# Performance work log

Hardware: AMD Instinct MI355X
Metric: run time of the kernel (lower is better)

## Reference

```python
import jax, jax.numpy as jnp
import numpy as np

B, S, F, D, H, L, NSUB, DFF = 64, 128, 62, 256, 4, 6, 32, 512
DH = D // 2           # each attention branch works on half of d_model
DEPTH = DH // H       # per-head dim = 32
NEG = -1000000000.0


def _rescale(w):
    # (1+e) / (1+exp(1-w))
    e1 = jnp.exp(jnp.float32(1.0))
    return (1.0 + e1) / (1.0 + jnp.exp(1.0 - w))


def _ln(x, g, b):
    mu = jnp.mean(x, -1, keepdims=True)
    v = jnp.var(x, -1, keepdims=True)
    return (x - mu) / jnp.sqrt(v + 1e-6) * g + b


def _heads(x, W, b):
    bsz, s, _ = x.shape
    return (x @ W + b).reshape(bsz, s, H, DEPTH).transpose(0, 2, 1, 3)  # (B,H,S,depth)


def setup_inputs():
    key = jax.random.key(0)
    ks = list(jax.random.split(key, 16))
    it = iter(ks)
    n = lambda shape: jax.random.normal(next(it), shape, jnp.float32) * 0.02
    inp = {
        "x": jax.random.normal(next(it), (B, S, F), jnp.float32),
        "adj_matrix": jax.random.normal(next(it), (B, S, S), jnp.float32),
        "dist_matrix": jax.random.uniform(next(it), (B, S, S), jnp.float32) * 10.0,
        "atom_match_matrix": jax.random.uniform(next(it), (B, NSUB, S), jnp.float32),
        "sum_atoms": jnp.ones((B, NSUB, 1), jnp.float32),
        "emb_W": n((F, D)), "emb_b": jnp.zeros((D,), jnp.float32),
        "glob_W": n((D, D)), "glob_b": jnp.zeros((D,), jnp.float32),
    }
    # per-layer params, stacked along leading L axis for lax.scan
    for p in ["Wq1", "Wk1", "Wv1", "Wo1", "Wq2", "Wk2", "Wv2", "Wo2"]:
        inp[p] = n((L, DH, DH))
    for p in ["bq1", "bk1", "bv1", "bo1", "bq2", "bk2", "bv2", "bo2"]:
        inp[p] = jnp.zeros((L, DH), jnp.float32)
    inp["Wf1"] = n((L, D, DFF)); inp["bf1"] = jnp.zeros((L, DFF), jnp.float32)
    inp["Wf2"] = n((L, DFF, D)); inp["bf2"] = jnp.zeros((L, D), jnp.float32)
    inp["g1"] = jnp.ones((L, D), jnp.float32); inp["be1"] = jnp.zeros((L, D), jnp.float32)
    inp["g2"] = jnp.ones((L, D), jnp.float32); inp["be2"] = jnp.zeros((L, D), jnp.float32)
    return inp


def reference(x, adj_matrix, dist_matrix, atom_match_matrix, sum_atoms,
              emb_W, emb_b, glob_W, glob_b,
              Wq1, Wk1, Wv1, Wo1, Wq2, Wk2, Wv2, Wo2,
              bq1, bk1, bv1, bo1, bq2, bk2, bv2, bo2,
              Wf1, bf1, Wf2, bf2, g1, be1, g2, be2):
    # padding mask from raw atom features: (B,1,1,S)
    mask = (jnp.sum(x, -1) == 0).astype(jnp.float32)[:, None, None, :]
    adj = adj_matrix[:, None]                  # (B,1,S,S) additive bias
    dist = _rescale(dist_matrix)[:, None]      # (B,1,S,S) multiplicative bias
    scale = 1.0 / jnp.sqrt(jnp.float32(DEPTH))

    h = jax.nn.relu(x @ emb_W + emb_b)         # embedding (eval mode, no dropout)

    def layer(h, p):
        (wq1, wk1, wv1, wo1, wq2, wk2, wv2, wo2,
         bq1_, bk1_, bv1_, bo1_, bq2_, bk2_, bv2_, bo2_,
         wf1, bf1_, wf2, bf2_, gg1, bb1, gg2, bb2) = p
        x1, x2 = jnp.split(h, 2, axis=-1)
        # local branch: plain scaled dot product + mask + adjacency bias
        Q = _heads(x1, wq1, bq1_); K = _heads(x1, wk1, bk1_); V = _heads(x1, wv1, bv1_)
        s = jnp.einsum('bhid,bhjd->bhij', Q, K) * scale + mask * NEG + adj
        o = jnp.einsum('bhij,bhjd->bhid', jax.nn.softmax(s, -1), V)
        x_l = o.transpose(0, 2, 1, 3).reshape(h.shape[0], S, DH) @ wo1 + bo1_
        # global branch: relu(QK^T) * rescaled_dist * scale + mask
        Q = _heads(x2, wq2, bq2_); K = _heads(x2, wk2, bk2_); V = _heads(x2, wv2, bv2_)
        s = jax.nn.relu(jnp.einsum('bhid,bhjd->bhij', Q, K)) * dist * scale + mask * NEG
        o = jnp.einsum('bhij,bhjd->bhid', jax.nn.softmax(s, -1), V)
        x_g = o.transpose(0, 2, 1, 3).reshape(h.shape[0], S, DH) @ wo2 + bo2_
        attn = jnp.concatenate([x_l, x_g], -1)
        out1 = _ln(h + attn, gg1, bb1)
        ffn = jax.nn.gelu(out1 @ wf1 + bf1_, approximate=False) @ wf2 + bf2_
        return _ln(ffn + out1, gg2, bb2), None

    xs = (Wq1, Wk1, Wv1, Wo1, Wq2, Wk2, Wv2, Wo2,
          bq1, bk1, bv1, bo1, bq2, bk2, bv2, bo2,
          Wf1, bf1, Wf2, bf2, g1, be1, g2, be2)
    h, _ = jax.lax.scan(layer, h, xs)

    pooled = (atom_match_matrix @ h) / sum_atoms      # (B,NSUB,D)
    out = jax.nn.relu(pooled @ glob_W + glob_b)
    return out
```

## Files before the change

kernel.cpp:

```cpp
#include <hip/hip_runtime.h>
#include <math.h>

#define B_ 64
#define S_ 128
#define F_ 62
#define D_ 256
#define H_ 4
#define L_ 6
#define NSUB_ 32
#define DFF_ 512
#define DH_ 128
#define DEPTH_ 32
#define MS_ (B_*S_)
#define NEGV (-1000000000.0f)
#define SCALE_ 0.17677669529663687f

typedef unsigned short u16;
typedef __attribute__((ext_vector_type(8))) short short8;
typedef __attribute__((ext_vector_type(4))) float f32x4;

__device__ __forceinline__ u16 f2b(float f){
  unsigned u = __float_as_uint(f);
  unsigned r = (u + 0x7fffu + ((u >> 16) & 1u)) >> 16;
  return (u16)r;
}

__device__ __forceinline__ void glds16(const void* g, void* l){
  __builtin_amdgcn_global_load_lds(
      (const __attribute__((address_space(1))) unsigned int*)g,
      (__attribute__((address_space(3))) unsigned int*)l, 16, 0, 0);
}

__global__ __launch_bounds__(256) void adjrescale_kernel(
    const float* __restrict__ adj, const float* __restrict__ dist,
    const float* __restrict__ maskb,
    float* __restrict__ adjm, float* __restrict__ distr){
  size_t i = (size_t)blockIdx.x*256 + threadIdx.x;
  int j = (int)(i & (S_-1));
  int b = (int)(i >> 14);
  const float e1 = 2.718281828459045f;
  distr[i] = (1.0f + e1) / (1.0f + expf(1.0f - dist[i])) * SCALE_;
  adjm[i]  = adj[i] + maskb[b*S_ + j];
}

struct TD { const float* src; u16* dst; int K, N, L; };
struct TDs { TD d[11]; };
__global__ __launch_bounds__(256) void transpose_all_kernel(TDs a){
  const TD p = a.d[blockIdx.z];
  int n0 = blockIdx.x*32, k0 = blockIdx.y*32;
  if(n0 >= p.N || k0 >= p.K) return;
  __shared__ float tbuf[32][33];
  int tx = threadIdx.x, ty = threadIdx.y;
  for(int l = 0; l < p.L; l++){
    const float* src = p.src + (size_t)l*p.K*p.N;
    u16* dst = p.dst + (size_t)l*p.K*p.N;
    #pragma unroll
    for(int i = 0; i < 4; i++)
      tbuf[ty + i*8][tx] = src[(size_t)(k0 + ty + i*8)*p.N + n0 + tx];
    __syncthreads();
    #pragma unroll
    for(int i = 0; i < 4; i++)
      dst[(size_t)(n0 + ty + i*8)*p.K + k0 + tx] = f2b(tbuf[tx][ty + i*8]);
    __syncthreads();
  }
}

__global__ __launch_bounds__(256) void embed_kernel(const float* __restrict__ x,
    const float* __restrict__ W, const float* __restrict__ bias,
    float* __restrict__ h, u16* __restrict__ h_bf, float* __restrict__ maskb){
  __shared__ float xs[4][F_];
  int r0 = blockIdx.x*4;
  int t = threadIdx.x;
  if(t < 4*F_){ int rr = t / F_, ff = t - rr*F_; xs[rr][ff] = x[(size_t)(r0+rr)*F_ + ff]; }
  __syncthreads();
  if(t < 4){
    float s = 0.f;
    #pragma unroll
    for(int f = 0; f < F_; f++) s += xs[t][f];
    maskb[r0 + t] = (s == 0.0f) ? NEGV : 0.0f;
  }
  float b = bias[t];
  float a0=b, a1=b, a2=b, a3=b;
  for(int k=0; k<F_; k++){
    float w = W[k*D_ + t];
    a0 = fmaf(xs[0][k], w, a0);
    a1 = fmaf(xs[1][k], w, a1);
    a2 = fmaf(xs[2][k], w, a2);
    a3 = fmaf(xs[3][k], w, a3);
  }
  a0 = fmaxf(a0, 0.f); a1 = fmaxf(a1, 0.f); a2 = fmaxf(a2, 0.f); a3 = fmaxf(a3, 0.f);
  h[(size_t)(r0+0)*D_ + t] = a0;  h_bf[(size_t)(r0+0)*D_ + t] = f2b(a0);
  h[(size_t)(r0+1)*D_ + t] = a1;  h_bf[(size_t)(r0+1)*D_ + t] = f2b(a1);
  h[(size_t)(r0+2)*D_ + t] = a2;  h_bf[(size_t)(r0+2)*D_ + t] = f2b(a2);
  h[(size_t)(r0+3)*D_ + t] = a3;  h_bf[(size_t)(r0+3)*D_ + t] = f2b(a3);
}

struct MG {
  const u16* A; const u16* W; const float* bias; void* C;
  int lda, K, ldc, aofs, cofs;
};
struct MG6 { MG g[6]; };

template<int TM, bool OUTBF, int ACT>
__global__ __launch_bounds__(256) void mgemm_kernel(MG6 args){
  const MG p = args.g[blockIdx.z];
  __shared__ u16 As[TM*32];
  __shared__ u16 Bs[128*32];
  const int t    = threadIdx.x;
  const int lane = t & 63;
  const int w    = t >> 6;
  const int ln   = lane & 15;
  const int qd   = lane >> 4;
  const int mw   = (w & 1) * (TM/2);
  const int nw   = (w >> 1) * 64;
  const int m0   = blockIdx.x * TM;
  const int n0   = blockIdx.y * 128;
  constexpr int MI = TM/32;
  f32x4 acc[MI][4];
  #pragma unroll
  for(int i=0;i<MI;i++)
    #pragma unroll
    for(int j=0;j<4;j++) acc[i][j] = (f32x4){0.f,0.f,0.f,0.f};

  const int srow = t >> 2;
  const int sc8  = (t & 3) * 8;

  for(int k0 = 0; k0 < p.K; k0 += 32){
    __syncthreads();
    glds16(p.A + (size_t)(m0 + srow)*p.lda + p.aofs + k0 + sc8, As + t*8);
    if(TM == 128)
      glds16(p.A + (size_t)(m0 + 64 + srow)*p.lda + p.aofs + k0 + sc8, As + (t+256)*8);
    glds16(p.W + (size_t)(n0 + srow)*p.K + k0 + sc8, Bs + t*8);
    glds16(p.W + (size_t)(n0 + 64 + srow)*p.K + k0 + sc8, Bs + (t+256)*8);
    __syncthreads();

    short8 a[MI], b[4];
    #pragma unroll
    for(int i=0;i<MI;i++) a[i] = *(const short8*)&As[(mw + i*16 + ln)*32 + qd*8];
    #pragma unroll
    for(int j=0;j<4;j++)  b[j] = *(const short8*)&Bs[(nw + j*16 + ln)*32 + qd*8];
    #pragma unroll
    for(int i=0;i<MI;i++)
      #pragma unroll
      for(int j=0;j<4;j++)
        acc[i][j] = __builtin_amdgcn_mfma_f32_16x16x32_bf16(a[i], b[j], acc[i][j], 0, 0, 0);
  }

  #pragma unroll
  for(int i=0;i<MI;i++){
    #pragma unroll
    for(int j=0;j<4;j++){
      int col = n0 + nw + j*16 + ln;
      float bv = p.bias[col];
      int rowb = m0 + mw + i*16 + qd*4;
      #pragma unroll
      for(int r=0;r<4;r++){
        float v = acc[i][j][r] + bv;
        if(ACT == 1) v = fmaxf(v, 0.f);
        if(ACT == 2) v = 0.5f*v*(1.0f + erff(v*0.70710678118654752f));
        size_t idx = (size_t)(rowb + r)*p.ldc + p.cofs + col;
        if(OUTBF) ((u16*)p.C)[idx] = f2b(v);
        else      ((float*)p.C)[idx] = v;
      }
    }
  }
}

struct QAArgs { const u16 *wq, *wk, *wv; const float *bq, *bk, *bv; };

__global__ __launch_bounds__(256) void qkv_attn_kernel(
    const u16* __restrict__ h_bf,
    QAArgs a1, QAArgs a2,
    const float* __restrict__ adjm, const float* __restrict__ distr,
    const float* __restrict__ maskb,
    u16* __restrict__ o1, u16* __restrict__ o2)
{
  __shared__ u16 SH[21760];
  u16* As = SH;
  u16* Bs = SH + 4096;
  u16* Qs = SH + 7168;
  u16* Ks = SH + 12288;
  u16* Vt = SH + 17408;
  u16* Ps = SH;

  const int bh = blockIdx.x;
  const int b  = bh >> 2;
  const int hh = bh & 3;
  const int branch = blockIdx.y;
  const QAArgs qa = branch ? a2 : a1;
  const u16* wqp = qa.wq + (size_t)hh*32*DH_;
  const u16* wkp = qa.wk + (size_t)hh*32*DH_;
  const u16* wvp = qa.wv + (size_t)hh*32*DH_;
  const int t = threadIdx.x;
  const int w = t >> 6, lane = t & 63;
  const int ln = lane & 15, qd = lane >> 4;
  const size_t rowbase = (size_t)b * S_;
  const int srow = t >> 2, sc8 = (t & 3) * 8;
  const int mbase = w * 32;

  float fix[2][4][8];
  {
    const float* basep = (branch ? distr : adjm) + rowbase*S_;
    #pragma unroll
    for(int mt = 0; mt < 2; mt++)
      #pragma unroll
      for(int r = 0; r < 4; r++){
        int row = mbase + mt*16 + qd*4 + r;
        #pragma unroll
        for(int nt = 0; nt < 8; nt++)
          fix[mt][r][nt] = basep[(size_t)row*S_ + nt*16 + ln];
      }
  }
  float mskv[8];
  if(branch){
    #pragma unroll
    for(int nt = 0; nt < 8; nt++) mskv[nt] = maskb[rowbase + nt*16 + ln];
  }

  f32x4 acc[2][6];
  #pragma unroll
  for(int i=0;i<2;i++)
    #pragma unroll
    for(int j=0;j<6;j++) acc[i][j] = (f32x4){0.f,0.f,0.f,0.f};

  for(int k0 = 0; k0 < DH_; k0 += 32){
    __syncthreads();
    glds16(h_bf + (rowbase + srow)*D_ + branch*DH_ + k0 + sc8, As + t*8);
    glds16(h_bf + (rowbase + 64 + srow)*D_ + branch*DH_ + k0 + sc8, As + (t+256)*8);
    {
      int r = t >> 2;
      const u16* wp = (r < 32) ? wqp : wkp;
      glds16(wp + (size_t)(r & 31)*DH_ + k0 + sc8, Bs + t*8);
    }
    if(t < 128){
      int c = 256 + t;
      glds16(wvp + (size_t)((c>>2) - 64)*DH_ + k0 + (c&3)*8, Bs + c*8);
    }
    __syncthreads();
    short8 av[2];
    #pragma unroll
    for(int mt = 0; mt < 2; mt++)
      av[mt] = *(const short8*)&As[(w*32 + mt*16 + ln)*32 + qd*8];
    #pragma unroll
    for(int nt = 0; nt < 6; nt++){
      short8 bv = *(const short8*)&Bs[(nt*16 + ln)*32 + qd*8];
      #pragma unroll
      for(int mt = 0; mt < 2; mt++)
        acc[mt][nt] = __builtin_amdgcn_mfma_f32_16x16x32_bf16(av[mt], bv, acc[mt][nt], 0, 0, 0);
    }
  }

  {
    const float* bqp = qa.bq + hh*32;
    const float* bkp = qa.bk + hh*32;
    const float* bvp = qa.bv + hh*32;
    #pragma unroll
    for(int mt = 0; mt < 2; mt++){
      int rb = w*32 + mt*16 + qd*4;
      #pragma unroll
      for(int j = 0; j < 2; j++){
        int d = j*16 + ln;
        float bq_ = bqp[d], bk_ = bkp[d], bv_ = bvp[d];
        #pragma unroll
        for(int r = 0; r < 4; r++){
          Qs[(rb+r)*40 + d]   = f2b(acc[mt][j][r]   + bq_);
          Ks[(rb+r)*40 + d]   = f2b(acc[mt][2+j][r] + bk_);
          Vt[d*136 + rb + r]  = f2b(acc[mt][4+j][r] + bv_);
        }
      }
    }
  }
  __syncthreads();

  short8 qf[2];
  #pragma unroll
  for(int mt = 0; mt < 2; mt++)
    qf[mt] = *(const short8*)&Qs[(mbase + mt*16 + ln)*40 + qd*8];
  short8 kf[8];
  #pragma unroll
  for(int nt = 0; nt < 8; nt++)
    kf[nt] = *(const short8*)&Ks[(nt*16 + ln)*40 + qd*8];
  __syncthreads();

  f32x4 sc[2][8];
  #pragma unroll
  for(int mt = 0; mt < 2; mt++)
    #pragma unroll
    for(int nt = 0; nt < 8; nt++)
      sc[mt][nt] = __builtin_amdgcn_mfma_f32_16x16x32_bf16(
          qf[mt], kf[nt], (f32x4){0.f,0.f,0.f,0.f}, 0, 0, 0);

  #pragma unroll
  for(int mt = 0; mt < 2; mt++){
    #pragma unroll
    for(int r = 0; r < 4; r++){
      #pragma unroll
      for(int nt = 0; nt < 8; nt++){
        float g = fix[mt][r][nt];
        float v;
        if(branch == 0) v = sc[mt][nt][r]*SCALE_ + g;
        else            v = fmaxf(sc[mt][nt][r], 0.f)*g + mskv[nt];
        sc[mt][nt][r] = v;
      }
    }
  }

  #pragma unroll
  for(int mt = 0; mt < 2; mt++){
    #pragma unroll
    for(int r = 0; r < 4; r++){
      float m = -3.4e38f;
      #pragma unroll
      for(int nt = 0; nt < 8; nt++) m = fmaxf(m, sc[mt][nt][r]);
      m = fmaxf(m, __shfl_xor(m, 1));
      m = fmaxf(m, __shfl_xor(m, 2));
      m = fmaxf(m, __shfl_xor(m, 4));
      m = fmaxf(m, __shfl_xor(m, 8));
      float sum = 0.f;
      float e[8];
      #pragma unroll
      for(int nt = 0; nt < 8; nt++){ e[nt] = __expf(sc[mt][nt][r] - m); sum += e[nt]; }
      sum += __shfl_xor(sum, 1);
      sum += __shfl_xor(sum, 2);
      sum += __shfl_xor(sum, 4);
      sum += __shfl_xor(sum, 8);
      float inv = 1.0f / sum;
      int row = mbase + mt*16 + qd*4 + r;
      #pragma unroll
      for(int nt = 0; nt < 8; nt++) Ps[row*136 + nt*16 + ln] = f2b(e[nt] * inv);
    }
  }

  f32x4 oacc[2][2];
  #pragma unroll
  for(int mt = 0; mt < 2; mt++)
    #pragma unroll
    for(int n2 = 0; n2 < 2; n2++) oacc[mt][n2] = (f32x4){0.f,0.f,0.f,0.f};
  #pragma unroll
  for(int kk = 0; kk < 4; kk++){
    short8 pa[2], vb[2];
    #pragma unroll
    for(int mt = 0; mt < 2; mt++)
      pa[mt] = *(const short8*)&Ps[(mbase + mt*16 + ln)*136 + kk*32 + qd*8];
    #pragma unroll
    for(int n2 = 0; n2 < 2; n2++)
      vb[n2] = *(const short8*)&Vt[(n2*16 + ln)*136 + kk*32 + qd*8];
    #pragma unroll
    for(int mt = 0; mt < 2; mt++)
      #pragma unroll
      for(int n2 = 0; n2 < 2; n2++)
        oacc[mt][n2] = __builtin_amdgcn_mfma_f32_16x16x32_bf16(pa[mt], vb[n2], oacc[mt][n2], 0, 0, 0);
  }

  u16* Og = branch ? o2 : o1;
  #pragma unroll
  for(int mt = 0; mt < 2; mt++){
    #pragma unroll
    for(int n2 = 0; n2 < 2; n2++){
      #pragma unroll
      for(int r = 0; r < 4; r++){
        int row = mbase + mt*16 + qd*4 + r;
        int d   = n2*16 + ln;
        Og[(rowbase + row)*DH_ + hh*DEPTH_ + d] = f2b(oacc[mt][n2][r]);
      }
    }
  }
}

struct TailArgs {
  const u16 *o1, *o2, *wo1, *wo2, *w1, *w2;
  const float *bo1, *bo2, *bf1, *bf2, *g1, *be1, *g2, *be2;
  float *h; u16 *h_bf;
};

__global__ __launch_bounds__(512) void tail_kernel(TailArgs p){
  __shared__ u16 X1[32*264];
  __shared__ u16 X2[32*520];
  __shared__ float redS[8][32], redQ[8][32];
  const int t = threadIdx.x;
  const int w = t >> 6, lane = t & 63;
  const int ln = lane & 15, qd = lane >> 4;
  const int m0 = blockIdx.x * 32;
  const int branch = w >> 2;
  const int c0 = w * 32;
  const int bc0 = (w & 3) * 32;

  const u16* Ao = branch ? p.o2 : p.o1;
  const u16* Wo = branch ? p.wo2 : p.wo1;
  const float* bo = branch ? p.bo2 : p.bo1;
  f32x4 y[2][2];
  #pragma unroll
  for(int mt=0;mt<2;mt++)
    #pragma unroll
    for(int nt=0;nt<2;nt++) y[mt][nt] = (f32x4){0.f,0.f,0.f,0.f};

  #pragma unroll
  for(int k0 = 0; k0 < DH_; k0 += 32){
    short8 af[2], bf[2];
    #pragma unroll
    for(int mt=0;mt<2;mt++)
      af[mt] = *(const short8*)(Ao + (size_t)(m0+mt*16+ln)*DH_ + k0 + qd*8);
    #pragma unroll
    for(int nt=0;nt<2;nt++)
      bf[nt] = *(const short8*)(Wo + (size_t)(bc0+nt*16+ln)*DH_ + k0 + qd*8);
    #pragma unroll
    for(int mt=0;mt<2;mt++)
      #pragma unroll
      for(int nt=0;nt<2;nt++)
        y[mt][nt] = __builtin_amdgcn_mfma_f32_16x16x32_bf16(af[mt], bf[nt], y[mt][nt], 0, 0, 0);
  }

  float sS[2][4] = {}, sQ[2][4] = {};
  #pragma unroll
  for(int mt=0;mt<2;mt++){
    #pragma unroll
    for(int nt=0;nt<2;nt++){
      int col = c0 + nt*16 + ln;
      float bv = bo[bc0 + nt*16 + ln];
      #pragma unroll
      for(int r=0;r<4;r++){
        float v = y[mt][nt][r] + bv + p.h[(size_t)(m0+mt*16+qd*4+r)*D_ + col];
        y[mt][nt][r] = v;
        sS[mt][r] += v;
        sQ[mt][r] += v*v;
      }
    }
  }
  #pragma unroll
  for(int mt=0;mt<2;mt++)
    #pragma unroll
    for(int r=0;r<4;r++){
      float a = sS[mt][r], b = sQ[mt][r];
      a += __shfl_xor(a,1); a += __shfl_xor(a,2); a += __shfl_xor(a,4); a += __shfl_xor(a,8);
      b += __shfl_xor(b,1); b += __shfl_xor(b,2); b += __shfl_xor(b,4); b += __shfl_xor(b,8);
      sS[mt][r] = a; sQ[mt][r] = b;
    }
  if(ln == 0){
    #pragma unroll
    for(int mt=0;mt<2;mt++)
      #pragma unroll
      for(int r=0;r<4;r++){
        int row = mt*16 + qd*4 + r;
        redS[w][row] = sS[mt][r];
        redQ[w][row] = sQ[mt][r];
      }
  }
  __syncthreads();
  float mu[2][4], iv[2][4];
  #pragma unroll
  for(int mt=0;mt<2;mt++)
    #pragma unroll
    for(int r=0;r<4;r++){
      int row = mt*16 + qd*4 + r;
      float s = 0.f, q = 0.f;
      #pragma unroll
      for(int ww=0;ww<8;ww++){ s += redS[ww][row]; q += redQ[ww][row]; }
      float m_ = s * (1.0f/D_);
      mu[mt][r] = m_;
      iv[mt][r] = rsqrtf(q*(1.0f/D_) - m_*m_ + 1e-6f);
    }
  #pragma unroll
  for(int mt=0;mt<2;mt++){
    #pragma unroll
    for(int nt=0;nt<2;nt++){
      int col = c0 + nt*16 + ln;
      float gg = p.g1[col], bb = p.be1[col];
      #pragma unroll
      for(int r=0;r<4;r++){
        float yy = (y[mt][nt][r] - mu[mt][r]) * iv[mt][r] * gg + bb;
        y[mt][nt][r] = yy;
        X1[(mt*16+qd*4+r)*264 + col] = f2b(yy);
      }
    }
  }
  __syncthreads();

  {
    const int fc0 = w * 64;
    f32x4 f1[2][4];
    #pragma unroll
    for(int mt=0;mt<2;mt++)
      #pragma unroll
      for(int nt=0;nt<4;nt++) f1[mt][nt] = (f32x4){0.f,0.f,0.f,0.f};
    for(int k0 = 0; k0 < D_; k0 += 32){
      short8 a0 = *(const short8*)&X1[(ln)*264 + k0 + qd*8];
      short8 a1 = *(const short8*)&X1[(16+ln)*264 + k0 + qd*8];
      #pragma unroll
      for(int nt=0;nt<4;nt++){
        short8 bfr = *(const short8*)(p.w1 + (size_t)(fc0+nt*16+ln)*D_ + k0 + qd*8);
        f1[0][nt] = __builtin_amdgcn_mfma_f32_16x16x32_bf16(a0, bfr, f1[0][nt], 0, 0, 0);
        f1[1][nt] = __builtin_amdgcn_mfma_f32_16x16x32_bf16(a1, bfr, f1[1][nt], 0, 0, 0);
      }
    }
    #pragma unroll
    for(int mt=0;mt<2;mt++){
      #pragma unroll
      for(int nt=0;nt<4;nt++){
        int col = fc0 + nt*16 + ln;
        float bv = p.bf1[col];
        #pragma unroll
        for(int r=0;r<4;r++){
          float v = f1[mt][nt][r] + bv;
          v = 0.5f*v*(1.0f + erff(v*0.70710678118654752f));
          X2[(mt*16+qd*4+r)*520 + col] = f2b(v);
        }
      }
    }
  }
  __syncthreads();

  f32x4 f2[2][2];
  #pragma unroll
  for(int mt=0;mt<2;mt++)
    #pragma unroll
    for(int nt=0;nt<2;nt++) f2[mt][nt] = (f32x4){0.f,0.f,0.f,0.f};
  for(int k0 = 0; k0 < DFF_; k0 += 32){
    short8 a0 = *(const short8*)&X2[(ln)*520 + k0 + qd*8];
    short8 a1 = *(const short8*)&X2[(16+ln)*520 + k0 + qd*8];
    #pragma unroll
    for(int nt=0;nt<2;nt++){
      short8 bfr = *(const short8*)(p.w2 + (size_t)(c0+nt*16+ln)*DFF_ + k0 + qd*8);
      f2[0][nt] = __builtin_amdgcn_mfma_f32_16x16x32_bf16(a0, bfr, f2[0][nt], 0, 0, 0);
      f2[1][nt] = __builtin_amdgcn_mfma_f32_16x16x32_bf16(a1, bfr, f2[1][nt], 0, 0, 0);
    }
  }
  float sS2[2][4] = {}, sQ2[2][4] = {};
  #pragma unroll
  for(int mt=0;mt<2;mt++){
    #pragma unroll
    for(int nt=0;nt<2;nt++){
      int col = c0 + nt*16 + ln;
      float bv = p.bf2[col];
      #pragma unroll
      for(int r=0;r<4;r++){
        float v = f2[mt][nt][r] + bv + y[mt][nt][r];
        f2[mt][nt][r] = v;
        sS2[mt][r] += v;
        sQ2[mt][r] += v*v;
      }
    }
  }
  #pragma unroll
  for(int mt=0;mt<2;mt++)
    #pragma unroll
    for(int r=0;r<4;r++){
      float a = sS2[mt][r], b = sQ2[mt][r];
      a += __shfl_xor(a,1); a += __shfl_xor(a,2); a += __shfl_xor(a,4); a += __shfl_xor(a,8);
      b += __shfl_xor(b,1); b += __shfl_xor(b,2); b += __shfl_xor(b,4); b += __shfl_xor(b,8);
      sS2[mt][r] = a; sQ2[mt][r] = b;
    }
  if(ln == 0){
    #pragma unroll
    for(int mt=0;mt<2;mt++)
      #pragma unroll
      for(int r=0;r<4;r++){
        int row = mt*16 + qd*4 + r;
        redS[w][row] = sS2[mt][r];
        redQ[w][row] = sQ2[mt][r];
      }
  }
  __syncthreads();
  #pragma unroll
  for(int mt=0;mt<2;mt++)
    #pragma unroll
    for(int r=0;r<4;r++){
      int row = mt*16 + qd*4 + r;
      float s = 0.f, q = 0.f;
      #pragma unroll
      for(int ww=0;ww<8;ww++){ s += redS[ww][row]; q += redQ[ww][row]; }
      float m_ = s * (1.0f/D_);
      mu[mt][r] = m_;
      iv[mt][r] = rsqrtf(q*(1.0f/D_) - m_*m_ + 1e-6f);
    }
  #pragma unroll
  for(int mt=0;mt<2;mt++){
    #pragma unroll
    for(int nt=0;nt<2;nt++){
      int col = c0 + nt*16 + ln;
      float gg = p.g2[col], bb = p.be2[col];
      #pragma unroll
      for(int r=0;r<4;r++){
        float yy = (f2[mt][nt][r] - mu[mt][r]) * iv[mt][r] * gg + bb;
        size_t idx = (size_t)(m0 + mt*16 + qd*4 + r)*D_ + col;
        p.h[idx] = yy;
        p.h_bf[idx] = f2b(yy);
      }
    }
  }
}

__global__ __launch_bounds__(256) void pool_kernel(
    const float* __restrict__ amm, const float* __restrict__ sum_atoms,
    const float* __restrict__ h, u16* __restrict__ pooled_bf)
{
  __shared__ float as[S_];
  int bn = blockIdx.x;
  int b  = bn >> 5;
  int t  = threadIdx.x;
  if(t < S_) as[t] = amm[(size_t)bn*S_ + t];
  __syncthreads();
  float acc = 0.f;
  const float* hb = h + (size_t)b*S_*D_ + t;
  #pragma unroll 4
  for(int s = 0; s < S_; s++) acc = fmaf(as[s], hb[(size_t)s*D_], acc);
  pooled_bf[(size_t)bn*D_ + t] = f2b(acc / sum_atoms[bn]);
}

extern "C" void kernel_launch(void* const* d_in, const int* in_sizes, int n_in,
                              void* d_out, int out_size, void* d_ws, size_t ws_size,
                              hipStream_t stream)
{
  const float* x     = (const float*)d_in[0];
  const float* adj   = (const float*)d_in[1];
  const float* dist  = (const float*)d_in[2];
  const float* amm   = (const float*)d_in[3];
  const float* sum_a = (const float*)d_in[4];
  const float* embW  = (const float*)d_in[5];
  const float* embB  = (const float*)d_in[6];
  const float* globW = (const float*)d_in[7];
  const float* globB = (const float*)d_in[8];
  const float* Wq1 = (const float*)d_in[9],  *Wk1 = (const float*)d_in[10],
             *Wv1 = (const float*)d_in[11], *Wo1 = (const float*)d_in[12],
             *Wq2 = (const float*)d_in[13], *Wk2 = (const float*)d_in[14],
             *Wv2 = (const float*)d_in[15], *Wo2 = (const float*)d_in[16];
  const float* bq1 = (const float*)d_in[17], *bk1 = (const float*)d_in[18],
             *bv1 = (const float*)d_in[19], *bo1 = (const float*)d_in[20],
             *bq2 = (const float*)d_in[21], *bk2 = (const float*)d_in[22],
             *bv2 = (const float*)d_in[23], *bo2 = (const float*)d_in[24];
  const float* Wf1 = (const float*)d_in[25], *bf1 = (const float*)d_in[26],
             *Wf2 = (const float*)d_in[27], *bf2 = (const float*)d_in[28],
             *g1  = (const float*)d_in[29], *be1 = (const float*)d_in[30],
             *g2  = (const float*)d_in[31], *be2 = (const float*)d_in[32];

  float* wsf = (float*)d_ws;
  float* h     = wsf; wsf += (size_t)MS_*D_;
  float* maskb = wsf; wsf += MS_;
  float* distr = wsf; wsf += (size_t)B_*S_*S_;
  float* adjm  = wsf; wsf += (size_t)B_*S_*S_;
  float* slab  = wsf; wsf += (size_t)MS_*DH_;
  u16* bb = (u16*)wsf;
  u16* h_bf    = bb; bb += (size_t)MS_*D_;
  u16* pooled_bf = bb; bb += (size_t)B_*NSUB_*D_;
  u16* globWt  = bb; bb += (size_t)D_*D_;
  u16* wq1t = bb; bb += (size_t)L_*DH_*DH_;
  u16* wk1t = bb; bb += (size_t)L_*DH_*DH_;
  u16* wv1t = bb; bb += (size_t)L_*DH_*DH_;
  u16* wo1t = bb; bb += (size_t)L_*DH_*DH_;
  u16* wq2t = bb; bb += (size_t)L_*DH_*DH_;
  u16* wk2t = bb; bb += (size_t)L_*DH_*DH_;
  u16* wv2t = bb; bb += (size_t)L_*DH_*DH_;
  u16* wo2t = bb; bb += (size_t)L_*DH_*DH_;
  u16* wf1t = bb; bb += (size_t)L_*D_*DFF_;
  u16* wf2t = bb; bb += (size_t)L_*DFF_*D_;
  u16* o1_bf = (u16*)slab;
  u16* o2_bf = o1_bf + (size_t)MS_*DH_;

  embed_kernel<<<MS_/4, 256, 0, stream>>>(x, embW, embB, h, h_bf, maskb);
  adjrescale_kernel<<<(B_*S_*S_)/256, 256, 0, stream>>>(adj, dist, maskb, adjm, distr);
  {
    TDs td;
    const float* S8[8] = {Wq1, Wk1, Wv1, Wo1, Wq2, Wk2, Wv2, Wo2};
    u16* D8[8] = {wq1t, wk1t, wv1t, wo1t, wq2t, wk2t, wv2t, wo2t};
    for(int i = 0; i < 8; i++) td.d[i] = {S8[i], D8[i], DH_, DH_, L_};
    td.d[8]  = {Wf1, wf1t, D_, DFF_, L_};
    td.d[9]  = {Wf2, wf2t, DFF_, D_, L_};
    td.d[10] = {globW, globWt, D_, D_, 1};
    transpose_all_kernel<<<dim3(16,16,11), dim3(32,8), 0, stream>>>(td);
  }

  for(int l = 0; l < L_; l++){
    QAArgs a1 = { wq1t + (size_t)l*DH_*DH_, wk1t + (size_t)l*DH_*DH_, wv1t + (size_t)l*DH_*DH_,
                  bq1 + (size_t)l*DH_, bk1 + (size_t)l*DH_, bv1 + (size_t)l*DH_ };
    QAArgs a2 = { wq2t + (size_t)l*DH_*DH_, wk2t + (size_t)l*DH_*DH_, wv2t + (size_t)l*DH_*DH_,
                  bq2 + (size_t)l*DH_, bk2 + (size_t)l*DH_, bv2 + (size_t)l*DH_ };
    qkv_attn_kernel<<<dim3(B_*H_, 2), 256, 0, stream>>>(h_bf, a1, a2, adjm, distr, maskb,
                                                        o1_bf, o2_bf);
    TailArgs ta;
    ta.o1 = o1_bf; ta.o2 = o2_bf;
    ta.wo1 = wo1t + (size_t)l*DH_*DH_; ta.wo2 = wo2t + (size_t)l*DH_*DH_;
    ta.w1 = wf1t + (size_t)l*D_*DFF_;  ta.w2 = wf2t + (size_t)l*DFF_*D_;
    ta.bo1 = bo1 + (size_t)l*DH_; ta.bo2 = bo2 + (size_t)l*DH_;
    ta.bf1 = bf1 + (size_t)l*DFF_; ta.bf2 = bf2 + (size_t)l*D_;
    ta.g1 = g1 + (size_t)l*D_; ta.be1 = be1 + (size_t)l*D_;
    ta.g2 = g2 + (size_t)l*D_; ta.be2 = be2 + (size_t)l*D_;
    ta.h = h; ta.h_bf = h_bf;
    tail_kernel<<<MS_/32, 512, 0, stream>>>(ta);
  }

  pool_kernel<<<B_*NSUB_, 256, 0, stream>>>(amm, sum_a, h, pooled_bf);
  {
    MG6 a;
    a.g[0].A = pooled_bf; a.g[0].W = globWt;
    a.g[0].bias = globB; a.g[0].C = (float*)d_out;
    a.g[0].lda = D_; a.g[0].K = D_; a.g[0].ldc = D_;
    a.g[0].aofs = 0; a.g[0].cofs = 0;
    mgemm_kernel<64,false,1><<<dim3((B_*NSUB_)/64, D_/128, 1), 256, 0, stream>>>(a);
  }
}
```

Baseline: 449.8 us.

## Store adj/dist bias as bf16 and stage full QKV projection operands at once

The precomputed adjacency+mask and rescaled distance matrices are now stored in bf16 instead of fp32, halving the bias traffic that every layer's attention kernel reads. The QKV projection now issues all four K-chunk loads into a larger shared buffer before a single barrier, replacing the per-chunk load/sync loop. Launch bounds now request two blocks per SM. This adds bf16 rounding to the additive adjacency term and the distance multiplier, which could affect accuracy, and the larger shared allocation may limit occupancy.

Result: faster. 434.4 us (-3.4%).

```diff
diff --git a/kernel.cpp b/kernel.cpp
--- a/kernel.cpp
+++ b/kernel.cpp
@@ -24,6 +24,9 @@
   unsigned r = (u + 0x7fffu + ((u >> 16) & 1u)) >> 16;
   return (u16)r;
 }
+__device__ __forceinline__ float b2f(u16 v){
+  return __uint_as_float((unsigned)v << 16);
+}
 
 __device__ __forceinline__ void glds16(const void* g, void* l){
   __builtin_amdgcn_global_load_lds(
@@ -34,13 +37,13 @@
 __global__ __launch_bounds__(256) void adjrescale_kernel(
     const float* __restrict__ adj, const float* __restrict__ dist,
     const float* __restrict__ maskb,
-    float* __restrict__ adjm, float* __restrict__ distr){
+    u16* __restrict__ adjm16, u16* __restrict__ distr16){
   size_t i = (size_t)blockIdx.x*256 + threadIdx.x;
   int j = (int)(i & (S_-1));
   int b = (int)(i >> 14);
   const float e1 = 2.718281828459045f;
-  distr[i] = (1.0f + e1) / (1.0f + expf(1.0f - dist[i])) * SCALE_;
-  adjm[i]  = adj[i] + maskb[b*S_ + j];
+  distr16[i] = f2b((1.0f + e1) / (1.0f + expf(1.0f - dist[i])) * SCALE_);
+  adjm16[i]  = f2b(adj[i] + maskb[b*S_ + j]);
 }
 
 struct TD { const float* src; u16* dst; int K, N, L; };
@@ -168,20 +171,20 @@
 
 struct QAArgs { const u16 *wq, *wk, *wv; const float *bq, *bk, *bv; };
 
-__global__ __launch_bounds__(256) void qkv_attn_kernel(
+__global__ __launch_bounds__(256, 2) void qkv_attn_kernel(
     const u16* __restrict__ h_bf,
     QAArgs a1, QAArgs a2,
-    const float* __restrict__ adjm, const float* __restrict__ distr,
+    const u16* __restrict__ adjm16, const u16* __restrict__ distr16,
     const float* __restrict__ maskb,
     u16* __restrict__ o1, u16* __restrict__ o2)
 {
-  __shared__ u16 SH[21760];
-  u16* As = SH;
-  u16* Bs = SH + 4096;
-  u16* Qs = SH + 7168;
-  u16* Ks = SH + 12288;
-  u16* Vt = SH + 17408;
-  u16* Ps = SH;
+  __shared__ u16 SH[32000];
+  u16* As4 = SH;
+  u16* Bs4 = SH + 16384;
+  u16* Ps  = SH;
+  u16* Qs  = SH + 17408;
+  u16* Ks  = SH + 22528;
+  u16* Vt  = SH + 27648;
 
   const int bh = blockIdx.x;
   const int b  = bh >> 2;
@@ -198,9 +201,9 @@
   const int srow = t >> 2, sc8 = (t & 3) * 8;
   const int mbase = w * 32;
 
-  float fix[2][4][8];
+  u16 fixu[2][4][8];
   {
-    const float* basep = (branch ? distr : adjm) + rowbase*S_;
+    const u16* basep = (branch ? distr16 : adjm16) + rowbase*S_;
     #pragma unroll
     for(int mt = 0; mt < 2; mt++)
       #pragma unroll
@@ -208,7 +211,7 @@
         int row = mbase + mt*16 + qd*4 + r;
         #pragma unroll
         for(int nt = 0; nt < 8; nt++)
-          fix[mt][r][nt] = basep[(size_t)row*S_ + nt*16 + ln];
+          fixu[mt][r][nt] = basep[(size_t)row*S_ + nt*16 + ln];
       }
   }
   float mskv[8];
@@ -217,38 +220,45 @@
     for(int nt = 0; nt < 8; nt++) mskv[nt] = maskb[rowbase + nt*16 + ln];
   }
 
-  f32x4 acc[2][6];
-  #pragma unroll
-  for(int i=0;i<2;i++)
-    #pragma unroll
-    for(int j=0;j<6;j++) acc[i][j] = (f32x4){0.f,0.f,0.f,0.f};
-
-  for(int k0 = 0; k0 < DH_; k0 += 32){
-    __syncthreads();
-    glds16(h_bf + (rowbase + srow)*D_ + branch*DH_ + k0 + sc8, As + t*8);
-    glds16(h_bf + (rowbase + 64 + srow)*D_ + branch*DH_ + k0 + sc8, As + (t+256)*8);
+  #pragma unroll
+  for(int kc = 0; kc < 4; kc++){
+    glds16(h_bf + (rowbase + srow)*D_ + branch*DH_ + kc*32 + sc8,
+           As4 + kc*4096 + t*8);
+    glds16(h_bf + (rowbase + 64 + srow)*D_ + branch*DH_ + kc*32 + sc8,
+           As4 + kc*4096 + (t+256)*8);
     {
       int r = t >> 2;
       const u16* wp = (r < 32) ? wqp : wkp;
-      glds16(wp + (size_t)(r & 31)*DH_ + k0 + sc8, Bs + t*8);
+      glds16(wp + (size_t)(r & 31)*DH_ + kc*32 + sc8, Bs4 + kc*3072 + t*8);
     }
     if(t < 128){
       int c = 256 + t;
-      glds16(wvp + (size_t)((c>>2) - 64)*DH_ + k0 + (c&3)*8, Bs + c*8);
-    }
-    __syncthreads();
+      glds16(wvp + (size_t)((c>>2) - 64)*DH_ + kc*32 + (c&3)*8, Bs4 + kc*3072 + c*8);
+    }
+  }
+  __syncthreads();
+
+  f32x4 acc[2][6];
+  #pragma unroll
+  for(int i=0;i<2;i++)
+    #pragma unroll
+    for(int j=0;j<6;j++) acc[i][j] = (f32x4){0.f,0.f,0.f,0.f};
+
+  #pragma unroll
+  for(int kc = 0; kc < 4; kc++){
     short8 av[2];
     #pragma unroll
     for(int mt = 0; mt < 2; mt++)
-      av[mt] = *(const short8*)&As[(w*32 + mt*16 + ln)*32 + qd*8];
+      av[mt] = *(const short8*)&As4[kc*4096 + (w*32 + mt*16 + ln)*32 + qd*8];
     #pragma unroll
     for(int nt = 0; nt < 6; nt++){
-      short8 bv = *(const short8*)&Bs[(nt*16 + ln)*32 + qd*8];
+      short8 bv = *(const short8*)&Bs4[kc*3072 + (nt*16 + ln)*32 + qd*8];
       #pragma unroll
       for(int mt = 0; mt < 2; mt++)
         acc[mt][nt] = __builtin_amdgcn_mfma_f32_16x16x32_bf16(av[mt], bv, acc[mt][nt], 0, 0, 0);
     }
   }
+  __syncthreads();
 
   {
     const float* bqp = qa.bq + hh*32;
@@ -280,7 +290,6 @@
   #pragma unroll
   for(int nt = 0; nt < 8; nt++)
     kf[nt] = *(const short8*)&Ks[(nt*16 + ln)*40 + qd*8];
-  __syncthreads();
 
   f32x4 sc[2][8];
   #pragma unroll
@@ -296,7 +305,7 @@
     for(int r = 0; r < 4; r++){
       #pragma unroll
       for(int nt = 0; nt < 8; nt++){
-        float g = fix[mt][r][nt];
+        float g = b2f(fixu[mt][r][nt]);
         float v;
         if(branch == 0) v = sc[mt][nt][r]*SCALE_ + g;
         else            v = fmaxf(sc[mt][nt][r], 0.f)*g + mskv[nt];
@@ -635,10 +644,11 @@
   float* wsf = (float*)d_ws;
   float* h     = wsf; wsf += (size_t)MS_*D_;
   float* maskb = wsf; wsf += MS_;
-  float* distr = wsf; wsf += (size_t)B_*S_*S_;
-  float* adjm  = wsf; wsf += (size_t)B_*S_*S_;
-  float* slab  = wsf; wsf += (size_t)MS_*DH_;
   u16* bb = (u16*)wsf;
+  u16* adjm16  = bb; bb += (size_t)B_*S_*S_;
+  u16* distr16 = bb; bb += (size_t)B_*S_*S_;
+  u16* o1_bf   = bb; bb += (size_t)MS_*DH_;
+  u16* o2_bf   = bb; bb += (size_t)MS_*DH_;
   u16* h_bf    = bb; bb += (size_t)MS_*D_;
   u16* pooled_bf = bb; bb += (size_t)B_*NSUB_*D_;
   u16* globWt  = bb; bb += (size_t)D_*D_;
@@ -652,11 +662,9 @@
   u16* wo2t = bb; bb += (size_t)L_*DH_*DH_;
   u16* wf1t = bb; bb += (size_t)L_*D_*DFF_;
   u16* wf2t = bb; bb += (size_t)L_*DFF_*D_;
-  u16* o1_bf = (u16*)slab;
-  u16* o2_bf = o1_bf + (size_t)MS_*DH_;
 
   embed_kernel<<<MS_/4, 256, 0, stream>>>(x, embW, embB, h, h_bf, maskb);
-  adjrescale_kernel<<<(B_*S_*S_)/256, 256, 0, stream>>>(adj, dist, maskb, adjm, distr);
+  adjrescale_kernel<<<(B_*S_*S_)/256, 256, 0, stream>>>(adj, dist, maskb, adjm16, distr16);
   {
     TDs td;
     const float* S8[8] = {Wq1, Wk1, Wv1, Wo1, Wq2, Wk2, Wv2, Wo2};
@@ -673,7 +681,7 @@
                   bq1 + (size_t)l*DH_, bk1 + (size_t)l*DH_, bv1 + (size_t)l*DH_ };
     QAArgs a2 = { wq2t + (size_t)l*DH_*DH_, wk2t + (size_t)l*DH_*DH_, wv2t + (size_t)l*DH_*DH_,
                   bq2 + (size_t)l*DH_, bk2 + (size_t)l*DH_, bv2 + (size_t)l*DH_ };
-    qkv_attn_kernel<<<dim3(B_*H_, 2), 256, 0, stream>>>(h_bf, a1, a2, adjm, distr, maskb,
+    qkv_attn_kernel<<<dim3(B_*H_, 2), 256, 0, stream>>>(h_bf, a1, a2, adjm16, distr16, maskb,
                                                         o1_bf, o2_bf);
     TailArgs ta;
     ta.o1 = o1_bf; ta.o2 = o2_bf;
```
